# Kernel tuning notes

Measured on AMD Instinct MI355X. Metric: run time of the kernel, lower is better.

The kernel has to match this reference:

```python
import jax, jax.numpy as jnp
import numpy as np

N_GRAPHS = 1024
NODES_PER_GRAPH = 512
N = N_GRAPHS * NODES_PER_GRAPH  # 524288 total nodes
HID = 256
EPS = 1e-6


def setup_inputs() -> dict:
    key = jax.random.key(0)
    k1, = jax.random.split(key, 1)
    tensor = jax.random.normal(k1, (N, HID), dtype=jnp.float32)
    batch_list = jnp.full((N_GRAPHS,), NODES_PER_GRAPH, dtype=jnp.int32)
    weight = jnp.ones((HID,), dtype=jnp.float32)
    bias = jnp.zeros((HID,), dtype=jnp.float32)
    mean_scale = jnp.ones((HID,), dtype=jnp.float32)
    return {"tensor": tensor, "batch_list": batch_list,
            "weight": weight, "bias": bias, "mean_scale": mean_scale}


def reference(tensor, batch_list, weight, bias, mean_scale):
    B = batch_list.shape[0]
    n = tensor.shape[0]
    # segment id per node: graph index repeated by per-graph node count
    seg = jnp.repeat(jnp.arange(B, dtype=jnp.int32), batch_list,
                     total_repeat_length=n)
    counts = batch_list.astype(tensor.dtype)[:, None]  # [B,1]
    # per-graph mean
    mean = jax.ops.segment_sum(tensor, seg, num_segments=B) / counts  # [B,HID]
    sub = tensor - mean[seg] * mean_scale                              # [N,HID]
    # per-graph (biased) std of the scaled-mean-subtracted features
    var = jax.ops.segment_sum(sub * sub, seg, num_segments=B) / counts
    std = jnp.sqrt(var + EPS)                                          # [B,HID]
    return weight * sub / std[seg] + bias
```

## Files before the change

### kernel.cpp

```cpp
#include <hip/hip_runtime.h>
#include <math.h>

#define HID      256
#define CHUNK    32
#define COLS     8
#define TPB      256
#define ROWGRPS  32
#define NPG      512
#define RPT      16
#define EPS_F    1e-6f

__global__ void scan_offsets(const int* __restrict__ bl, int B, int* __restrict__ offs) {
    __shared__ int s[1024];
    const int t = threadIdx.x;
    const int v = (t < B) ? bl[t] : 0;
    s[t] = v;
    __syncthreads();
    int acc = v;
    for (int d = 1; d < 1024; d <<= 1) {
        const int add = (t >= d) ? s[t - d] : 0;
        __syncthreads();
        acc += add;
        s[t] = acc;
        __syncthreads();
    }
    if (t < B) offs[t] = acc - v;
}

__global__ __launch_bounds__(TPB, 2)
void graphnorm_kernel(const float* __restrict__ x,
                      const int*   __restrict__ offs,
                      const int*   __restrict__ bl,
                      const float* __restrict__ w,
                      const float* __restrict__ bias,
                      const float* __restrict__ ms,
                      float*       __restrict__ out) {
    const int blk = blockIdx.x;
    const int g   = blk >> 3;
    const int c   = blk & 7;
    const int f0  = c * CHUNK;
    const int t   = threadIdx.x;
    const int col = t & (COLS - 1);
    const int rg  = t >> 3;

    const int   off     = offs[g];
    const float cnt     = (float)bl[g];
    const float inv_cnt = 1.0f / cnt;

    const size_t rowbase = (size_t)(off + rg * RPT) * HID + (size_t)(f0 + col * 4);
    const float* __restrict__ px = x + rowbase;

    float4 v[RPT];
#pragma unroll
    for (int k = 0; k < RPT; ++k)
        v[k] = *reinterpret_cast<const float4*>(px + (size_t)k * HID);

    float4 s1 = make_float4(0.f, 0.f, 0.f, 0.f);
    float4 s2 = make_float4(0.f, 0.f, 0.f, 0.f);
#pragma unroll
    for (int k = 0; k < RPT; ++k) {
        s1.x += v[k].x; s1.y += v[k].y; s1.z += v[k].z; s1.w += v[k].w;
        s2.x += v[k].x * v[k].x; s2.y += v[k].y * v[k].y;
        s2.z += v[k].z * v[k].z; s2.w += v[k].w * v[k].w;
    }

    __shared__ float4 red1[ROWGRPS][COLS + 1];
    __shared__ float4 red2[ROWGRPS][COLS + 1];
    red1[rg][col] = s1;
    red2[rg][col] = s2;
    __syncthreads();
#pragma unroll
    for (int st = ROWGRPS / 2; st >= 1; st >>= 1) {
        if (rg < st) {
            float4 a1 = red1[rg + st][col];
            float4 a2 = red2[rg + st][col];
            float4 b1 = red1[rg][col];
            float4 b2 = red2[rg][col];
            b1.x += a1.x; b1.y += a1.y; b1.z += a1.z; b1.w += a1.w;
            b2.x += a2.x; b2.y += a2.y; b2.z += a2.z; b2.w += a2.w;
            red1[rg][col] = b1;
            red2[rg][col] = b2;
        }
        __syncthreads();
    }

    __shared__ float4 sh_mu[COLS], sh_a[COLS], sh_b[COLS];
    if (t < COLS) {
        const float4 S1 = red1[0][t];
        const float4 S2 = red2[0][t];
        const int f = f0 + t * 4;
        const float4 wv = *reinterpret_cast<const float4*>(w + f);
        const float4 bv = *reinterpret_cast<const float4*>(bias + f);
        const float4 mv = *reinterpret_cast<const float4*>(ms + f);
        float4 mu, a;
        {
            const float m   = S1.x * inv_cnt;
            const float var = S2.x * inv_cnt - m * m * mv.x * (2.0f - mv.x);
            mu.x = m * mv.x;  a.x = wv.x * rsqrtf(var + EPS_F);
        }
        {
            const float m   = S1.y * inv_cnt;
            const float var = S2.y * inv_cnt - m * m * mv.y * (2.0f - mv.y);
            mu.y = m * mv.y;  a.y = wv.y * rsqrtf(var + EPS_F);
        }
        {
            const float m   = S1.z * inv_cnt;
            const float var = S2.z * inv_cnt - m * m * mv.z * (2.0f - mv.z);
            mu.z = m * mv.z;  a.z = wv.z * rsqrtf(var + EPS_F);
        }
        {
            const float m   = S1.w * inv_cnt;
            const float var = S2.w * inv_cnt - m * m * mv.w * (2.0f - mv.w);
            mu.w = m * mv.w;  a.w = wv.w * rsqrtf(var + EPS_F);
        }
        sh_mu[t] = mu; sh_a[t] = a; sh_b[t] = bv;
    }
    __syncthreads();

    const float4 mu = sh_mu[col];
    const float4 a  = sh_a[col];
    const float4 bb = sh_b[col];

    float* __restrict__ po = out + rowbase;
#pragma unroll
    for (int k = 0; k < RPT; ++k) {
        float4 o;
        o.x = (v[k].x - mu.x) * a.x + bb.x;
        o.y = (v[k].y - mu.y) * a.y + bb.y;
        o.z = (v[k].z - mu.z) * a.z + bb.z;
        o.w = (v[k].w - mu.w) * a.w + bb.w;
        *reinterpret_cast<float4*>(po + (size_t)k * HID) = o;
    }
}

extern "C" void kernel_launch(void* const* d_in, const int* in_sizes, int n_in,
                              void* d_out, int out_size, void* d_ws, size_t ws_size,
                              hipStream_t stream) {
    const float* x    = (const float*)d_in[0];
    const int*   bl   = (const int*)d_in[1];
    const float* w    = (const float*)d_in[2];
    const float* bias = (const float*)d_in[3];
    const float* ms   = (const float*)d_in[4];
    float*       out  = (float*)d_out;

    const int B = in_sizes[1];
    int* offs = (int*)d_ws;

    scan_offsets<<<1, 1024, 0, stream>>>(bl, B, offs);

    const int n_blocks = B * (HID / CHUNK);
    graphnorm_kernel<<<n_blocks, TPB, 0, stream>>>(x, offs, bl, w, bias, ms, out);
}
```

Measured before the change: 860.5 us.

## Split into stats and normalize kernels with fixed graph size and fused affine

Replaces the single fused kernel, which kept each block's 32-column by 512-row slice in registers, with two passes. A stats kernel computes per-graph scale and shift coefficients using full contiguous rows per block, and a separate normalize kernel reads x again and applies one FMA per element. The goal is fully coalesced 1KB-row accesses and cheaper reductions, and the prefix-scan launch is removed. The cost is a second full read of x, which adds HBM traffic. It also hardcodes 512 nodes per graph, ignoring the batch_list offsets.

```diff
diff --git a/kernel.cpp b/kernel.cpp
--- a/kernel.cpp
+++ b/kernel.cpp
@@ -1,135 +1,122 @@
 #include <hip/hip_runtime.h>
 #include <math.h>
 
-#define HID      256
-#define CHUNK    32
-#define COLS     8
-#define TPB      256
-#define ROWGRPS  32
-#define NPG      512
-#define RPT      16
-#define EPS_F    1e-6f
+#define HID    256
+#define H4     64
+#define NPG    512
+#define EPS_F  1e-6f
 
-__global__ void scan_offsets(const int* __restrict__ bl, int B, int* __restrict__ offs) {
-    __shared__ int s[1024];
-    const int t = threadIdx.x;
-    const int v = (t < B) ? bl[t] : 0;
-    s[t] = v;
-    __syncthreads();
-    int acc = v;
-    for (int d = 1; d < 1024; d <<= 1) {
-        const int add = (t >= d) ? s[t - d] : 0;
-        __syncthreads();
-        acc += add;
-        s[t] = acc;
-        __syncthreads();
-    }
-    if (t < B) offs[t] = acc - v;
-}
+__global__ __launch_bounds__(256, 4)
+void stats_kernel(const float* __restrict__ x,
+                  const int*   __restrict__ bl,
+                  const float* __restrict__ w,
+                  const float* __restrict__ bias,
+                  const float* __restrict__ ms,
+                  float*       __restrict__ aA,
+                  float*       __restrict__ cA)
+{
+    const int g  = blockIdx.x;
+    const int t  = threadIdx.x;
+    const int f4 = t & (H4 - 1);
+    const int p  = t >> 6;
 
-__global__ __launch_bounds__(TPB, 2)
-void graphnorm_kernel(const float* __restrict__ x,
-                      const int*   __restrict__ offs,
-                      const int*   __restrict__ bl,
-                      const float* __restrict__ w,
-                      const float* __restrict__ bias,
-                      const float* __restrict__ ms,
-                      float*       __restrict__ out) {
-    const int blk = blockIdx.x;
-    const int g   = blk >> 3;
-    const int c   = blk & 7;
-    const int f0  = c * CHUNK;
-    const int t   = threadIdx.x;
-    const int col = t & (COLS - 1);
-    const int rg  = t >> 3;
-
-    const int   off     = offs[g];
-    const float cnt     = (float)bl[g];
-    const float inv_cnt = 1.0f / cnt;
-
-    const size_t rowbase = (size_t)(off + rg * RPT) * HID + (size_t)(f0 + col * 4);
-    const float* __restrict__ px = x + rowbase;
-
-    float4 v[RPT];
-#pragma unroll
-    for (int k = 0; k < RPT; ++k)
-        v[k] = *reinterpret_cast<const float4*>(px + (size_t)k * HID);
+    const float4* __restrict__ x4 =
+        reinterpret_cast<const float4*>(x) +
+        (size_t)g * NPG * H4 + (size_t)p * H4 + f4;
 
     float4 s1 = make_float4(0.f, 0.f, 0.f, 0.f);
     float4 s2 = make_float4(0.f, 0.f, 0.f, 0.f);
-#pragma unroll
-    for (int k = 0; k < RPT; ++k) {
-        s1.x += v[k].x; s1.y += v[k].y; s1.z += v[k].z; s1.w += v[k].w;
-        s2.x += v[k].x * v[k].x; s2.y += v[k].y * v[k].y;
-        s2.z += v[k].z * v[k].z; s2.w += v[k].w * v[k].w;
+#pragma unroll 8
+    for (int i = 0; i < NPG / 4; ++i) {
+        const float4 v = x4[(size_t)i * 4 * H4];
+        s1.x += v.x; s1.y += v.y; s1.z += v.z; s1.w += v.w;
+        s2.x = fmaf(v.x, v.x, s2.x);
+        s2.y = fmaf(v.y, v.y, s2.y);
+        s2.z = fmaf(v.z, v.z, s2.z);
+        s2.w = fmaf(v.w, v.w, s2.w);
     }
 
-    __shared__ float4 red1[ROWGRPS][COLS + 1];
-    __shared__ float4 red2[ROWGRPS][COLS + 1];
-    red1[rg][col] = s1;
-    red2[rg][col] = s2;
+    __shared__ float4 sh1[4][H4];
+    __shared__ float4 sh2[4][H4];
+    sh1[p][f4] = s1;
+    sh2[p][f4] = s2;
     __syncthreads();
+
+    if (t < H4) {
+        float4 S1 = sh1[0][t];
+        float4 S2 = sh2[0][t];
 #pragma unroll
-    for (int st = ROWGRPS / 2; st >= 1; st >>= 1) {
-        if (rg < st) {
-            float4 a1 = red1[rg + st][col];
-            float4 a2 = red2[rg + st][col];
-            float4 b1 = red1[rg][col];
-            float4 b2 = red2[rg][col];
-            b1.x += a1.x; b1.y += a1.y; b1.z += a1.z; b1.w += a1.w;
-            b2.x += a2.x; b2.y += a2.y; b2.z += a2.z; b2.w += a2.w;
-            red1[rg][col] = b1;
-            red2[rg][col] = b2;
+        for (int q = 1; q < 4; ++q) {
+            const float4 a1 = sh1[q][t];
+            const float4 a2 = sh2[q][t];
+            S1.x += a1.x; S1.y += a1.y; S1.z += a1.z; S1.w += a1.w;
+            S2.x += a2.x; S2.y += a2.y; S2.z += a2.z; S2.w += a2.w;
         }
-        __syncthreads();
-    }
-
-    __shared__ float4 sh_mu[COLS], sh_a[COLS], sh_b[COLS];
-    if (t < COLS) {
-        const float4 S1 = red1[0][t];
-        const float4 S2 = red2[0][t];
-        const int f = f0 + t * 4;
-        const float4 wv = *reinterpret_cast<const float4*>(w + f);
+        const float inv = 1.0f / (float)bl[g];
+        const int   f   = t * 4;
+        const float4 wv = *reinterpret_cast<const float4*>(w    + f);
         const float4 bv = *reinterpret_cast<const float4*>(bias + f);
-        const float4 mv = *reinterpret_cast<const float4*>(ms + f);
-        float4 mu, a;
+        const float4 mv = *reinterpret_cast<const float4*>(ms   + f);
+        float4 av, cv;
         {
-            const float m   = S1.x * inv_cnt;
-            const float var = S2.x * inv_cnt - m * m * mv.x * (2.0f - mv.x);
-            mu.x = m * mv.x;  a.x = wv.x * rsqrtf(var + EPS_F);
+            const float m   = S1.x * inv;
+            const float var = S2.x * inv - m * m * mv.x * (2.0f - mv.x);
+            const float a   = wv.x * rsqrtf(var + EPS_F);
+            av.x = a;  cv.x = bv.x - m * mv.x * a;
         }
         {
-            const float m   = S1.y * inv_cnt;
-            const float var = S2.y * inv_cnt - m * m * mv.y * (2.0f - mv.y);
-            mu.y = m * mv.y;  a.y = wv.y * rsqrtf(var + EPS_F);
+            const float m   = S1.y * inv;
+            const float var = S2.y * inv - m * m * mv.y * (2.0f - mv.y);
+            const float a   = wv.y * rsqrtf(var + EPS_F);
+            av.y = a;  cv.y = bv.y - m * mv.y * a;
         }
         {
-            const float m   = S1.z * inv_cnt;
-            const float var = S2.z * inv_cnt - m * m * mv.z * (2.0f - mv.z);
-            mu.z = m * mv.z;  a.z = wv.z * rsqrtf(var + EPS_F);
+            const float m   = S1.z * inv;
+            const float var = S2.z * inv - m * m * mv.z * (2.0f - mv.z);
+            const float a   = wv.z * rsqrtf(var + EPS_F);
+            av.z = a;  cv.z = bv.z - m * mv.z * a;
         }
         {
-            const float m   = S1.w * inv_cnt;
-            const float var = S2.w * inv_cnt - m * m * mv.w * (2.0f - mv.w);
-            mu.w = m * mv.w;  a.w = wv.w * rsqrtf(var + EPS_F);
+            const float m   = S1.w * inv;
+            const float var = S2.w * inv - m * m * mv.w * (2.0f - mv.w);
+            const float a   = wv.w * rsqrtf(var + EPS_F);
+            av.w = a;  cv.w = bv.w - m * mv.w * a;
         }
-        sh_mu[t] = mu; sh_a[t] = a; sh_b[t] = bv;
+        reinterpret_cast<float4*>(aA)[(size_t)g * H4 + t] = av;
+        reinterpret_cast<float4*>(cA)[(size_t)g * H4 + t] = cv;
     }
-    __syncthreads();
+}
 
-    const float4 mu = sh_mu[col];
-    const float4 a  = sh_a[col];
-    const float4 bb = sh_b[col];
+#define RPB 64
+__global__ __launch_bounds__(256, 4)
+void norm_kernel(const float* __restrict__ x,
+                 const float* __restrict__ aA,
+                 const float* __restrict__ cA,
+                 float*       __restrict__ out)
+{
+    const int t  = threadIdx.x;
+    const int f4 = t & (H4 - 1);
+    const int p  = t >> 6;
+    const size_t row0 = (size_t)blockIdx.x * RPB;
+    const int g  = (int)(row0 / NPG);
 
-    float* __restrict__ po = out + rowbase;
+    const float4 a = reinterpret_cast<const float4*>(aA)[(size_t)g * H4 + f4];
+    const float4 c = reinterpret_cast<const float4*>(cA)[(size_t)g * H4 + f4];
+
+    const float4* __restrict__ xi =
+        reinterpret_cast<const float4*>(x)   + (row0 + p) * H4 + f4;
+    float4* __restrict__ oi =
+        reinterpret_cast<float4*>(out)       + (row0 + p) * H4 + f4;
+
 #pragma unroll
-    for (int k = 0; k < RPT; ++k) {
+    for (int i = 0; i < RPB / 4; ++i) {
+        const float4 v = xi[(size_t)i * 4 * H4];
         float4 o;
-        o.x = (v[k].x - mu.x) * a.x + bb.x;
-        o.y = (v[k].y - mu.y) * a.y + bb.y;
-        o.z = (v[k].z - mu.z) * a.z + bb.z;
-        o.w = (v[k].w - mu.w) * a.w + bb.w;
-        *reinterpret_cast<float4*>(po + (size_t)k * HID) = o;
+        o.x = fmaf(v.x, a.x, c.x);
+        o.y = fmaf(v.y, a.y, c.y);
+        o.z = fmaf(v.z, a.z, c.z);
+        o.w = fmaf(v.w, a.w, c.w);
+        oi[(size_t)i * 4 * H4] = o;
     }
 }
 
@@ -144,10 +131,12 @@
     float*       out  = (float*)d_out;
 
     const int B = in_sizes[1];
-    int* offs = (int*)d_ws;
+    float* aA = (float*)d_ws;
+    float* cA = aA + (size_t)B * HID;
 
-    scan_offsets<<<1, 1024, 0, stream>>>(bl, B, offs);
+    stats_kernel<<<B, 256, 0, stream>>>(x, bl, w, bias, ms, aA, cA);
 
-    const int n_blocks = B * (HID / CHUNK);
-    graphnorm_kernel<<<n_blocks, TPB, 0, stream>>>(x, offs, bl, w, bias, ms, out);
+    const int n_rows   = B * NPG;
+    const int n_blocks = n_rows / RPB;
+    norm_kernel<<<n_blocks, 256, 0, stream>>>(x, aA, cA, out);
 }
```

Result: slower. 962.1 us (+11.8%).
